# Kernel optimization log

Hardware: AMD Instinct MI355X
Metric: run time of the kernel (lower is better)

## Reference

```python
import jax, jax.numpy as jnp
import numpy as np

# qshift_a: Kingsbury 10-tap Q-shift filters (sum(h0a) = sqrt(2)).
_H0A = np.array([0.0351638365171441, 0.0, -0.0883294244510729,
                 0.233890320607236, 0.760272369066126, 0.587518297723561,
                 0.0, -0.114301837144249, 0.0, 0.0], dtype=np.float64)
_H0B = _H0A[::-1].copy()
_ALT = (-1.0) ** np.arange(10)
_H1A = _H0B * _ALT            # highpass tree a
_H1B = _H1A[::-1].copy()
# synthesis filters (g0a = h0b, g0b = h0a, g1a = h1b, g1b = h1a)
G0A = _H0B.astype(np.float32)
G0B = _H0A.astype(np.float32)
G1A = _H1B.astype(np.float32)
G1B = _H1A.astype(np.float32)


def _reflect(x, minx, maxx):
    # dtcwt symmetric-extension index reflection (static, numpy)
    x = np.asarray(x, dtype=np.float64)
    rng = maxx - minx
    rng2 = 2.0 * rng
    mod = np.fmod(x - minx, rng2)
    normed = np.where(mod < 0, mod + rng2, mod)
    out = np.where(normed >= rng, rng2 - normed, normed) + minx
    return out.astype(np.int64)


def _colifilt(X, ha, hb):
    # X: (B, C, r, c) -> (B, C, 2r, c). ha, hb are 1-D numpy filters (static).
    m = ha.shape[0]
    m2 = m // 2
    assert m2 % 2 == 1, 'implemented for 10/14/18-tap qshift (m/2 odd)'
    b, ch, r, c = X.shape
    r2 = r // 2
    xe = _reflect(np.arange(-m2, r + m2), -0.5, r - 0.5)   # static indices
    t = np.arange(2, r + m - 1, 2)
    if float(np.sum(ha * hb)) > 0:
        ta, tb = t, t - 1
    else:
        ta, tb = t - 1, t
    Xa = X[:, :, xe[ta], :]   # (B, C, r/2 + m/2 - 1, c)
    Xb = X[:, :, xe[tb], :]
    hao, hae = ha[0::2], ha[1::2]
    hbo, hbe = hb[0::2], hb[1::2]

    def vconv(Z, h):
        # valid convolution along dim 2 (true conv: filter flipped)
        hf = h[::-1]
        out = Z[:, :, 0:r2, :] * float(hf[0])
        for k in range(1, m2):
            out = out + Z[:, :, k:k + r2, :] * float(hf[k])
        return out

    y = jnp.stack([vconv(Xb, hao), vconv(Xa, hbo),
                   vconv(Xb, hae), vconv(Xa, hbe)], axis=3)  # (B,C,r/2,4,c)
    return y.reshape(b, ch, 2 * r, c)


def _rowifilt(X, ha, hb):
    return jnp.swapaxes(_colifilt(jnp.swapaxes(X, 2, 3), ha, hb), 2, 3)


def _c2q(wr, wi):
    # complex pair of subbands -> real quad image. wr, wi: (B, C, 2, H, W) -> (B, C, 2H, 2W)
    w1r, w2r = wr[:, :, 0], wr[:, :, 1]
    w1i, w2i = wi[:, :, 0], wi[:, :, 1]
    x1 = w1r + w2r
    x2 = w1i + w2i
    x3 = w1i - w2i
    x4 = w2r - w1r
    b, c, h, w = x1.shape
    top = jnp.stack([x1, x2], axis=-1).reshape(b, c, h, 2 * w)
    bot = jnp.stack([x3, x4], axis=-1).reshape(b, c, h, 2 * w)
    y = jnp.stack([top, bot], axis=-2).reshape(b, c, 2 * h, 2 * w)
    return y * np.float32(1.0 / np.sqrt(2.0))


def setup_inputs() -> dict:
    key = jax.random.key(0)
    k1, k2, k3 = jax.random.split(key, 3)
    B, C, H, W = 8, 64, 128, 128
    Yl = jax.random.normal(k1, (B, C, H, W), dtype=jnp.float32)
    Yhr = jax.random.normal(k2, (B, C, 6, H // 2, W // 2), dtype=jnp.float32)
    Yhi = jax.random.normal(k3, (B, C, 6, H // 2, W // 2), dtype=jnp.float32)
    return {"Yl": Yl, "Yhr": Yhr, "Yhi": Yhi}


def reference(Yl, Yhr, Yhi):
    lh = _c2q(Yhr[:, :, 0:6:5], Yhi[:, :, 0:6:5])
    hl = _c2q(Yhr[:, :, 2:4:1], Yhi[:, :, 2:4:1])
    hh = _c2q(Yhr[:, :, 1:5:3], Yhi[:, :, 1:5:3])
    y1 = _rowifilt(Yl, G0B, G0A) + _rowifilt(hl, G1B, G1A)
    y2 = _rowifilt(lh, G0B, G0A) + _rowifilt(hh, G1B, G1A)
    return _colifilt(y1, G0B, G0A) + _colifilt(y2, G1B, G1A)
```

## Files before the change

### kernel.cpp

```cpp
#include <hip/hip_runtime.h>

#define NTHREADS 256
#define YROWS 40
#define ICOLS 40
#define TILE_C 64

__device__ __forceinline__ int reflect128(int p) {
    p = (p < 0) ? (-p - 1) : p;
    p = (p >= 128) ? (255 - p) : p;
    return p;
}

__device__ __forceinline__ void load_w(int j, float* w0, float* w1) {
    const float A =  0.0351638365171441f;
    const float B = -0.0883294244510729f;
    const float C =  0.233890320607236f;
    const float D =  0.760272369066126f;
    const float E =  0.587518297723561f;
    const float F = -0.114301837144249f;
    if (j == 0) {
        w0[0]=0.f; w0[1]=0.f; w0[2]=D;  w0[3]=B;  w0[4]=A;
        w1[0]=0.f; w1[1]=C;   w1[2]=E;  w1[3]=F;  w1[4]=0.f;
    } else if (j == 1) {
        w0[0]=0.f; w0[1]=C;   w0[2]=E;  w0[3]=F;  w0[4]=0.f;
        w1[0]=0.f; w1[1]=0.f; w1[2]=-D; w1[3]=-B; w1[4]=-A;
    } else if (j == 2) {
        w0[0]=0.f; w0[1]=F;   w0[2]=E;  w0[3]=C;  w0[4]=0.f;
        w1[0]=-A;  w1[1]=-B;  w1[2]=-D; w1[3]=0.f; w1[4]=0.f;
    } else {
        w0[0]=A;   w0[1]=B;   w0[2]=D;  w0[3]=0.f; w0[4]=0.f;
        w1[0]=0.f; w1[1]=F;   w1[2]=E;  w1[3]=C;  w1[4]=0.f;
    }
}

__global__ __launch_bounds__(NTHREADS)
void dtcwt_inv_kernel(const float* __restrict__ Yl,
                      const float* __restrict__ Yhr,
                      const float* __restrict__ Yhi,
                      float* __restrict__ out)
{
    const int tid   = threadIdx.x;
    const int ct    = blockIdx.x;
    const int rt    = blockIdx.y;
    const int plane = blockIdx.z;

    const int OR0 = rt * 64;
    const int OC0 = ct * 64;
    const int i0r = OR0 >> 2;
    const int i0c = OC0 >> 2;
    const int yrb = 2 * i0r - 4;
    const int icb = 2 * i0c - 4;

    const float* yl = Yl + (size_t)plane * (128 * 128);
    const size_t sb = (size_t)plane * 6 * 4096;

    __shared__ float sYl[YROWS][ICOLS];
    __shared__ float sLh[YROWS][ICOLS];
    __shared__ float sHl[YROWS][ICOLS];
    __shared__ float sHh[YROWS][ICOLS];
    __shared__ float sY1[YROWS][TILE_C];
    __shared__ float sY2[YROWS][TILE_C];

    const float RS2 = 0.70710678118654752440f;
    for (int e = tid; e < YROWS * ICOLS; e += NTHREADS) {
        const int t = e / ICOLS;
        const int u = e - t * ICOLS;
        const int ry = reflect128(yrb + t);
        const int ic = reflect128(icb + u);
        sYl[t][u] = yl[ry * 128 + ic];

        const int p = ry & 1, q = ic & 1;
        const int off = (ry >> 1) * 64 + (ic >> 1);
        const float* src = (p == q) ? (Yhr + sb) : (Yhi + sb);
        const float sA = (p == 1 && q == 1) ? -RS2 : RS2;
        const float sB = (p == 1 && q == 0) ? -RS2 : RS2;
        float a0 = src[0 * 4096 + off], b0 = src[5 * 4096 + off];
        float a1 = src[2 * 4096 + off], b1 = src[3 * 4096 + off];
        float a2 = src[1 * 4096 + off], b2 = src[4 * 4096 + off];
        sLh[t][u] = sA * a0 + sB * b0;
        sHl[t][u] = sA * a1 + sB * b1;
        sHh[t][u] = sA * a2 + sB * b2;
    }
    __syncthreads();

    const int c  = tid & 63;
    const int jc = c & 3;
    float w0c[5], w1c[5];
    load_w(jc, w0c, w1c);
    const int base0 = 2 * (c >> 2) + (jc & 1);
    const int base1 = 2 * (c >> 2) + ((jc & 1) ^ 1);

    for (int t = tid >> 6; t < YROWS; t += 4) {
        float acc1 = 0.f, acc2 = 0.f;
#pragma unroll
        for (int k = 0; k < 5; ++k) {
            acc1 += sYl[t][base0 + 2 * k] * w0c[k];
            acc1 += sHl[t][base1 + 2 * k] * w1c[k];
            acc2 += sLh[t][base0 + 2 * k] * w0c[k];
            acc2 += sHh[t][base1 + 2 * k] * w1c[k];
        }
        sY1[t][c] = acc1;
        sY2[t][c] = acc2;
    }
    __syncthreads();

    const int j = tid >> 6;
    float w0o[5], w1o[5];
    load_w(j, w0o, w1o);
    const int p0 = j & 1;
    const int p1 = p0 ^ 1;

#pragma unroll
    for (int m = 0; m < 16; ++m) {
        float acc = 0.f;
#pragma unroll
        for (int k = 0; k < 5; ++k) {
            acc += sY1[2 * m + p0 + 2 * k][c] * w0o[k];
            acc += sY2[2 * m + p1 + 2 * k][c] * w1o[k];
        }
        const int orow = OR0 + 4 * m + j;
        out[((size_t)plane * 256 + orow) * 256 + OC0 + c] = acc;
    }
}

extern "C" void kernel_launch(void* const* d_in, const int* in_sizes, int n_in,
                              void* d_out, int out_size, void* d_ws, size_t ws_size,
                              hipStream_t stream) {
    const float* Yl  = (const float*)d_in[0];
    const float* Yhr = (const float*)d_in[1];
    const float* Yhi = (const float*)d_in[2];
    float* out = (float*)d_out;

    const int planes = in_sizes[0] / (128 * 128);
    dim3 grid(4, 4, planes);
    dtcwt_inv_kernel<<<grid, NTHREADS, 0, stream>>>(Yl, Yhr, Yhi, out);
}
```

Baseline: 297.8 us.

## Drop zero taps, split shared tiles by parity, store intermediates as bf16

Rewrites the fused inverse DTCWT kernel. Each polyphase filter is reduced to its three nonzero taps, with the taps and offsets kept in constant memory. Shared tiles are split by column and row parity so the taps read contiguous entries. High-pass coefficients are loaded once per 2x2 quad, and all 12 subband values are reused across the four outputs. The row-pass intermediates are stored in shared memory as bfloat16, which loses precision and may fail the accuracy tolerance. The launch-bounds occupancy hint is also raised.

```diff
diff --git a/kernel.cpp b/kernel.cpp
--- a/kernel.cpp
+++ b/kernel.cpp
@@ -1,39 +1,33 @@
 #include <hip/hip_runtime.h>
+#include <hip/hip_bf16.h>
 
 #define NTHREADS 256
-#define YROWS 40
-#define ICOLS 40
-#define TILE_C 64
 
 __device__ __forceinline__ int reflect128(int p) {
     p = (p < 0) ? (-p - 1) : p;
     p = (p >= 128) ? (255 - p) : p;
     return p;
 }
-
-__device__ __forceinline__ void load_w(int j, float* w0, float* w1) {
-    const float A =  0.0351638365171441f;
-    const float B = -0.0883294244510729f;
-    const float C =  0.233890320607236f;
-    const float D =  0.760272369066126f;
-    const float E =  0.587518297723561f;
-    const float F = -0.114301837144249f;
-    if (j == 0) {
-        w0[0]=0.f; w0[1]=0.f; w0[2]=D;  w0[3]=B;  w0[4]=A;
-        w1[0]=0.f; w1[1]=C;   w1[2]=E;  w1[3]=F;  w1[4]=0.f;
-    } else if (j == 1) {
-        w0[0]=0.f; w0[1]=C;   w0[2]=E;  w0[3]=F;  w0[4]=0.f;
-        w1[0]=0.f; w1[1]=0.f; w1[2]=-D; w1[3]=-B; w1[4]=-A;
-    } else if (j == 2) {
-        w0[0]=0.f; w0[1]=F;   w0[2]=E;  w0[3]=C;  w0[4]=0.f;
-        w1[0]=-A;  w1[1]=-B;  w1[2]=-D; w1[3]=0.f; w1[4]=0.f;
-    } else {
-        w0[0]=A;   w0[1]=B;   w0[2]=D;  w0[3]=0.f; w0[4]=0.f;
-        w1[0]=0.f; w1[1]=F;   w1[2]=E;  w1[3]=C;  w1[4]=0.f;
-    }
+__device__ __forceinline__ int reflect64(int p) {
+    p = (p < 0) ? (-p - 1) : p;
+    p = (p >= 64) ? (127 - p) : p;
+    return p;
 }
 
-__global__ __launch_bounds__(NTHREADS)
+__constant__ int   cs0[4] = {2, 1, 1, 0};
+__constant__ int   cs1[4] = {1, 2, 0, 1};
+__constant__ float cc0[4][3] = {
+    { 0.760272369066126f, -0.0883294244510729f,  0.0351638365171441f},
+    { 0.233890320607236f,  0.587518297723561f,  -0.114301837144249f},
+    {-0.114301837144249f,  0.587518297723561f,   0.233890320607236f},
+    { 0.0351638365171441f, -0.0883294244510729f, 0.760272369066126f}};
+__constant__ float cc1[4][3] = {
+    { 0.233890320607236f,  0.587518297723561f,  -0.114301837144249f},
+    {-0.760272369066126f,  0.0883294244510729f, -0.0351638365171441f},
+    {-0.0351638365171441f, 0.0883294244510729f, -0.760272369066126f},
+    {-0.114301837144249f,  0.587518297723561f,   0.233890320607236f}};
+
+__global__ __launch_bounds__(NTHREADS, 4)
 void dtcwt_inv_kernel(const float* __restrict__ Yl,
                       const float* __restrict__ Yhr,
                       const float* __restrict__ Yhi,
@@ -44,82 +38,101 @@
     const int rt    = blockIdx.y;
     const int plane = blockIdx.z;
 
-    const int OR0 = rt * 64;
-    const int OC0 = ct * 64;
-    const int i0r = OR0 >> 2;
-    const int i0c = OC0 >> 2;
+    const int OR0 = rt * 64, OC0 = ct * 64;
+    const int i0r = OR0 >> 2, i0c = OC0 >> 2;
     const int yrb = 2 * i0r - 4;
     const int icb = 2 * i0c - 4;
 
     const float* yl = Yl + (size_t)plane * (128 * 128);
-    const size_t sb = (size_t)plane * 6 * 4096;
+    const float* hr = Yhr + (size_t)plane * 6 * 4096;
+    const float* hi = Yhi + (size_t)plane * 6 * 4096;
 
-    __shared__ float sYl[YROWS][ICOLS];
-    __shared__ float sLh[YROWS][ICOLS];
-    __shared__ float sHl[YROWS][ICOLS];
-    __shared__ float sHh[YROWS][ICOLS];
-    __shared__ float sY1[YROWS][TILE_C];
-    __shared__ float sY2[YROWS][TILE_C];
+    __shared__ float sYl[2][40][20];
+    __shared__ float sLh[2][40][20];
+    __shared__ float sHl[2][40][20];
+    __shared__ float sHh[2][40][20];
+    __shared__ __hip_bfloat16 sY1[2][20][64];
+    __shared__ __hip_bfloat16 sY2[2][20][64];
 
     const float RS2 = 0.70710678118654752440f;
-    for (int e = tid; e < YROWS * ICOLS; e += NTHREADS) {
-        const int t = e / ICOLS;
-        const int u = e - t * ICOLS;
+
+    for (int e = tid; e < 1600; e += NTHREADS) {
+        const int t = e / 40;
+        const int u = e - t * 40;
         const int ry = reflect128(yrb + t);
         const int ic = reflect128(icb + u);
-        sYl[t][u] = yl[ry * 128 + ic];
+        sYl[u & 1][t][u >> 1] = yl[ry * 128 + ic];
+    }
 
-        const int p = ry & 1, q = ic & 1;
-        const int off = (ry >> 1) * 64 + (ic >> 1);
-        const float* src = (p == q) ? (Yhr + sb) : (Yhi + sb);
-        const float sA = (p == 1 && q == 1) ? -RS2 : RS2;
-        const float sB = (p == 1 && q == 0) ? -RS2 : RS2;
-        float a0 = src[0 * 4096 + off], b0 = src[5 * 4096 + off];
-        float a1 = src[2 * 4096 + off], b1 = src[3 * 4096 + off];
-        float a2 = src[1 * 4096 + off], b2 = src[4 * 4096 + off];
-        sLh[t][u] = sA * a0 + sB * b0;
-        sHl[t][u] = sA * a1 + sB * b1;
-        sHh[t][u] = sA * a2 + sB * b2;
+    for (int e = tid; e < 400; e += NTHREADS) {
+        const int t2 = e / 20;
+        const int u2 = e - t2 * 20;
+        const int r2 = reflect64(i0r - 2 + t2);
+        const int c2 = reflect64(i0c - 2 + u2);
+        const int off = r2 * 64 + c2;
+        float ar0 = hr[0 * 4096 + off], ar1 = hr[1 * 4096 + off], ar2 = hr[2 * 4096 + off];
+        float ar3 = hr[3 * 4096 + off], ar4 = hr[4 * 4096 + off], ar5 = hr[5 * 4096 + off];
+        float ai0 = hi[0 * 4096 + off], ai1 = hi[1 * 4096 + off], ai2 = hi[2 * 4096 + off];
+        float ai3 = hi[3 * 4096 + off], ai4 = hi[4 * 4096 + off], ai5 = hi[5 * 4096 + off];
+#pragma unroll
+        for (int dt = 0; dt < 2; ++dt) {
+#pragma unroll
+            for (int du = 0; du < 2; ++du) {
+                const int t = 2 * t2 + dt, u = 2 * u2 + du;
+                const int p = reflect128(yrb + t) & 1;
+                const int q = reflect128(icb + u) & 1;
+                const float sA = (p & q) ? -RS2 : RS2;
+                const float sB = (p & ~q & 1) ? -RS2 : RS2;
+                float b0, b5, b2v, b3, b1, b4;
+                if (p == q) { b0 = ar0; b5 = ar5; b2v = ar2; b3 = ar3; b1 = ar1; b4 = ar4; }
+                else        { b0 = ai0; b5 = ai5; b2v = ai2; b3 = ai3; b1 = ai1; b4 = ai4; }
+                sLh[du][t][u2] = sA * b0 + sB * b5;
+                sHl[du][t][u2] = sA * b2v + sB * b3;
+                sHh[du][t][u2] = sA * b1 + sB * b4;
+            }
+        }
     }
     __syncthreads();
 
     const int c  = tid & 63;
     const int jc = c & 3;
-    float w0c[5], w1c[5];
-    load_w(jc, w0c, w1c);
-    const int base0 = 2 * (c >> 2) + (jc & 1);
-    const int base1 = 2 * (c >> 2) + ((jc & 1) ^ 1);
+    const int pc0 = jc & 1;
+    const int pc1 = pc0 ^ 1;
+    const int h0 = (c >> 2) + cs0[jc];
+    const int h1 = (c >> 2) + cs1[jc];
+    const float a0 = cc0[jc][0], a1 = cc0[jc][1], a2 = cc0[jc][2];
+    const float b0w = cc1[jc][0], b1w = cc1[jc][1], b2w = cc1[jc][2];
 
-    for (int t = tid >> 6; t < YROWS; t += 4) {
-        float acc1 = 0.f, acc2 = 0.f;
-#pragma unroll
-        for (int k = 0; k < 5; ++k) {
-            acc1 += sYl[t][base0 + 2 * k] * w0c[k];
-            acc1 += sHl[t][base1 + 2 * k] * w1c[k];
-            acc2 += sLh[t][base0 + 2 * k] * w0c[k];
-            acc2 += sHh[t][base1 + 2 * k] * w1c[k];
-        }
-        sY1[t][c] = acc1;
-        sY2[t][c] = acc2;
+    for (int t = tid >> 6; t < 40; t += 4) {
+        const float* yl0 = &sYl[pc0][t][h0];
+        const float* hl1 = &sHl[pc1][t][h1];
+        const float* lh0 = &sLh[pc0][t][h0];
+        const float* hh1 = &sHh[pc1][t][h1];
+        float acc1 = yl0[0] * a0 + yl0[1] * a1 + yl0[2] * a2
+                   + hl1[0] * b0w + hl1[1] * b1w + hl1[2] * b2w;
+        float acc2 = lh0[0] * a0 + lh0[1] * a1 + lh0[2] * a2
+                   + hh1[0] * b0w + hh1[1] * b1w + hh1[2] * b2w;
+        sY1[t & 1][t >> 1][c] = __float2bfloat16(acc1);
+        sY2[t & 1][t >> 1][c] = __float2bfloat16(acc2);
     }
     __syncthreads();
 
-    const int j = tid >> 6;
-    float w0o[5], w1o[5];
-    load_w(j, w0o, w1o);
-    const int p0 = j & 1;
-    const int p1 = p0 ^ 1;
+    const int j  = tid >> 6;
+    const int p0 = j & 1, p1 = p0 ^ 1;
+    const int g0 = cs0[j], g1 = cs1[j];
+    const float d0 = cc0[j][0], d1 = cc0[j][1], d2 = cc0[j][2];
+    const float e0 = cc1[j][0], e1 = cc1[j][1], e2 = cc1[j][2];
 
+    float* orow = out + ((size_t)plane * 256 + OR0 + j) * 256 + OC0 + c;
 #pragma unroll
     for (int m = 0; m < 16; ++m) {
-        float acc = 0.f;
-#pragma unroll
-        for (int k = 0; k < 5; ++k) {
-            acc += sY1[2 * m + p0 + 2 * k][c] * w0o[k];
-            acc += sY2[2 * m + p1 + 2 * k][c] * w1o[k];
-        }
-        const int orow = OR0 + 4 * m + j;
-        out[((size_t)plane * 256 + orow) * 256 + OC0 + c] = acc;
+        float acc = __bfloat162float(sY1[p0][m + g0][c]) * d0
+                  + __bfloat162float(sY1[p0][m + g0 + 1][c]) * d1
+                  + __bfloat162float(sY1[p0][m + g0 + 2][c]) * d2
+                  + __bfloat162float(sY2[p1][m + g1][c]) * e0
+                  + __bfloat162float(sY2[p1][m + g1 + 1][c]) * e1
+                  + __bfloat162float(sY2[p1][m + g1 + 2][c]) * e2;
+        orow[(size_t)(4 * m) * 256] = acc;
     }
 }
 
```

New measurement: 276.8 us. 1.08x faster.
